# Optimization experiments

Measured on AMD Instinct MI355X. Metric: run time of the kernel, lower is better.

## Reference

```python
import jax, jax.numpy as jnp
import numpy as np

D = 1024
H = 16
S = 2048
B = 4
DF = 4 * D
EPS = 1e-5


def setup_inputs() -> dict:
    key = jax.random.key(0)
    ks = jax.random.split(key, 12)
    sd = 0.02
    return {
        "x": jax.random.normal(ks[0], (B, S, D), dtype=jnp.float32),
        "Wq": jax.random.normal(ks[1], (D, D), dtype=jnp.float32) * sd,
        "Wk": jax.random.normal(ks[2], (D, D), dtype=jnp.float32) * sd,
        "Wv": jax.random.normal(ks[3], (D, D), dtype=jnp.float32) * sd,
        "Wo": jax.random.normal(ks[4], (D, D), dtype=jnp.float32) * sd,
        "bo": jnp.zeros((D,), dtype=jnp.float32),
        "W1": jax.random.normal(ks[5], (D, DF), dtype=jnp.float32) * sd,
        "b1": jnp.zeros((DF,), dtype=jnp.float32),
        "W2": jax.random.normal(ks[6], (DF, D), dtype=jnp.float32) * sd,
        "b2": jnp.zeros((D,), dtype=jnp.float32),
        "g1": jnp.ones((D,), dtype=jnp.float32),
        "s1": jnp.zeros((D,), dtype=jnp.float32),
        "g2": jnp.ones((D,), dtype=jnp.float32),
        "s2": jnp.zeros((D,), dtype=jnp.float32),
    }


def _gelu(x):
    # tanh approximation exactly as in the torch GELU module
    c = jnp.sqrt(jnp.asarray(2.0 / jnp.pi, dtype=x.dtype))
    return 0.5 * x * (1.0 + jnp.tanh(c * (x + 0.044715 * x ** 3)))


def _layernorm(x, scale, shift):
    mean = jnp.mean(x, axis=-1, keepdims=True)
    var = jnp.var(x, axis=-1, keepdims=True)  # biased, as unbiased=False
    return scale * (x - mean) * jax.lax.rsqrt(var + EPS) + shift


def _attention(x, Wq, Wk, Wv, Wo, bo):
    b, s, d = x.shape
    hd = d // H
    q = (x @ Wq).reshape(b, s, H, hd).transpose(0, 2, 1, 3)  # [b,h,s,hd]
    k = (x @ Wk).reshape(b, s, H, hd).transpose(0, 2, 1, 3)
    v = (x @ Wv).reshape(b, s, H, hd).transpose(0, 2, 1, 3)
    scores = jnp.einsum("bhqd,bhkd->bhqk", q, k) / jnp.sqrt(jnp.asarray(hd, x.dtype))
    mask = jnp.triu(jnp.ones((s, s), dtype=bool), k=1)
    scores = jnp.where(mask, -jnp.inf, scores)
    w = jax.nn.softmax(scores, axis=-1)  # dropout is identity (rate=0 / eval)
    ctx = jnp.einsum("bhqk,bhkd->bhqd", w, v)
    ctx = ctx.transpose(0, 2, 1, 3).reshape(b, s, d)
    return ctx @ Wo + bo


def reference(x, Wq, Wk, Wv, Wo, bo, W1, b1, W2, b2, g1, s1, g2, s2):
    h = x + _attention(_layernorm(x, g1, s1), Wq, Wk, Wv, Wo, bo)
    y = _layernorm(h, g2, s2)
    ff = _gelu(y @ W1 + b1) @ W2 + b2
    return h + ff
```

## Files before the change

### kernel.cpp

```cpp
#include <hip/hip_runtime.h>
#include <hip/hip_bf16.h>

#define DEV __device__ __forceinline__

typedef __bf16 bf16x8 __attribute__((ext_vector_type(8)));
typedef __bf16 bf16x2v __attribute__((ext_vector_type(2)));
typedef float f32x4 __attribute__((ext_vector_type(4)));
typedef float f32x16 __attribute__((ext_vector_type(16)));
typedef unsigned int u32;
typedef unsigned int u32x4 __attribute__((ext_vector_type(4)));
typedef __hip_bfloat16 hbf;

constexpr int Dm = 1024;
constexpr int Hh = 16;
constexpr int Ss = 2048;
constexpr int Bb = 4;
constexpr int DFm = 4096;
constexpr int LDQ = 3072;

DEV unsigned short f2bfu(float f) {
  hbf h = __float2bfloat16(f);
  return __builtin_bit_cast(unsigned short, h);
}

DEV float bfu2f(unsigned short u) { return __builtin_bit_cast(float, (u32)u << 16); }

DEV u32 pkbf(float x, float y) {
  bf16x2v v = {(__bf16)x, (__bf16)y};
  return __builtin_bit_cast(u32, v);
}

DEV float gelu_f(float x) {
  float e = __expf(-1.5957691216057308f * (x + 0.044715f * x * x * x));
  return x * __builtin_amdgcn_rcpf(1.f + e);
}

template <int N>
DEV void s_vmcnt() {
  if constexpr (N == 0) asm volatile("s_waitcnt vmcnt(0)" ::: "memory");
  else if constexpr (N == 5) asm volatile("s_waitcnt vmcnt(5)" ::: "memory");
  else if constexpr (N == 6) asm volatile("s_waitcnt vmcnt(6)" ::: "memory");
  else if constexpr (N == 8) asm volatile("s_waitcnt vmcnt(8)" ::: "memory");
  else static_assert(N == 0, "unsupported vmcnt");
}

#define GLDS(src, dst)                                                                     \
  __builtin_amdgcn_global_load_lds((const __attribute__((address_space(1))) void*)(src),   \
                                   (__attribute__((address_space(3))) void*)(dst), 16, 0, 0)

__global__ __launch_bounds__(256) void wtransall_kernel(
    const float* __restrict__ Wq, const float* __restrict__ Wk,
    const float* __restrict__ Wv, const float* __restrict__ Wo,
    const float* __restrict__ W1, const float* __restrict__ W2,
    hbf* __restrict__ dqkv, hbf* __restrict__ dwo,
    hbf* __restrict__ dw1, hbf* __restrict__ dw2) {
  __shared__ float tile[32][33];
  const int i = blockIdx.x;
  const float* W;
  hbf* Wt;
  int K, N, k0, n0;
  if (i < 4096) {
    int z = i >> 10, j = i & 1023;
    W = z == 0 ? Wq : z == 1 ? Wk : z == 2 ? Wv : Wo;
    Wt = z == 3 ? dwo : dqkv + (size_t)z * 1024 * 1024;
    K = 1024; N = 1024; k0 = (j & 31) * 32; n0 = (j >> 5) * 32;
  } else if (i < 8192) {
    int j = i - 4096;
    W = W1; Wt = dw1; K = 1024; N = 4096;
    k0 = (j & 31) * 32; n0 = (j >> 5) * 32;
  } else {
    int j = i - 8192;
    W = W2; Wt = dw2; K = 4096; N = 1024;
    k0 = (j & 127) * 32; n0 = (j >> 7) * 32;
  }
  int tx = threadIdx.x & 31, ty = threadIdx.x >> 5;
  for (int r = ty; r < 32; r += 8) tile[r][tx] = W[(size_t)(k0 + r) * N + n0 + tx];
  __syncthreads();
  for (int r = ty; r < 32; r += 8)
    Wt[(size_t)(n0 + r) * K + k0 + tx] = __float2bfloat16(tile[tx][r]);
}

template <bool INBF>
__global__ __launch_bounds__(256) void ln_kernel(const void* __restrict__ xv,
                                                 const float* __restrict__ g,
                                                 const float* __restrict__ b,
                                                 hbf* __restrict__ y) {
  int row = ((blockIdx.x & 7) << 10) | (blockIdx.x >> 3);
  int t = threadIdx.x;
  float4 v;
  if constexpr (INBF) {
    ushort4 u = ((const ushort4*)((const hbf*)xv + (size_t)row * Dm))[t];
    v.x = bfu2f(u.x); v.y = bfu2f(u.y); v.z = bfu2f(u.z); v.w = bfu2f(u.w);
  } else {
    v = ((const float4*)((const float*)xv + (size_t)row * Dm))[t];
  }
  float s = v.x + v.y + v.z + v.w;
  float q = v.x * v.x + v.y * v.y + v.z * v.z + v.w * v.w;
#pragma unroll
  for (int off = 32; off > 0; off >>= 1) {
    s += __shfl_down(s, off);
    q += __shfl_down(q, off);
  }
  __shared__ float red[10];
  int wave = t >> 6, lane = t & 63;
  if (lane == 0) { red[wave] = s; red[4 + wave] = q; }
  __syncthreads();
  if (t == 0) {
    float ts = red[0] + red[1] + red[2] + red[3];
    float tq = red[4] + red[5] + red[6] + red[7];
    float mean = ts * (1.f / Dm);
    float var = tq * (1.f / Dm) - mean * mean;
    red[8] = mean;
    red[9] = rsqrtf(var + 1e-5f);
  }
  __syncthreads();
  float mean = red[8], inv = red[9];
  float4 gv = ((const float4*)g)[t];
  float4 bv = ((const float4*)b)[t];
  ushort4 o;
  o.x = f2bfu(gv.x * (v.x - mean) * inv + bv.x);
  o.y = f2bfu(gv.y * (v.y - mean) * inv + bv.y);
  o.z = f2bfu(gv.z * (v.z - mean) * inv + bv.z);
  o.w = f2bfu(gv.w * (v.w - mean) * inv + bv.w);
  ((ushort4*)(y + (size_t)row * Dm))[t] = o;
}

template <int BM, int BN, int WM, int WN, int NTHR, int NPH, int ACT, bool HAS_BIAS, int RES,
          bool OUT_BF16>
__global__ __launch_bounds__(NTHR, 2) void gemm8(const hbf* __restrict__ A,
                                                 const hbf* __restrict__ Bt,
                                                 void* __restrict__ Cv,
                                                 const float* __restrict__ bias,
                                                 const void* __restrict__ resv,
                                                 int M, int N, int K) {
  constexpr int MR = (BM / WM) / 16, NR = (BN / WN) / 16;
  constexpr int MQ = MR / 2, NQ = NR / 2;
  constexpr int RPA = (BM / WM) / 2;
  constexpr int RPB = (BN / WN) / 2;
  constexpr int ASL = (BM / 2) * 64;
  constexpr int BSL = (BN / 2) * 64;
  constexpr int PERBUF = 2 * ASL + 2 * BSL;
  constexpr int ALD = ASL / (8 * NTHR);
  constexpr int BLD = BSL / (8 * NTHR);
  constexpr int VPB = 2 * ALD + BLD;
  constexpr int VP4 = 2 * ALD + 2 * BLD;

  __shared__ __align__(16) hbf lds[2 * PERBUF];

  const int tid = threadIdx.x;
  const int lane = tid & 63, wave = tid >> 6;
  const int wr = wave / WN, wc = wave % WN;
  const int lr = lane & 15, lg = lane >> 4;

  const int xcd = blockIdx.x & 7, oidx = blockIdx.x >> 3;
  const int gsup = oidx >> 6, r6 = oidx & 63;
  const int m0 = (xcd * 8 + (r6 >> 3)) * BM;
  const int n0 = (gsup * 8 + (r6 & 7)) * BN;

  const hbf* Ab = A + (size_t)m0 * K;
  const hbf* Bb = Bt + (size_t)n0 * K;

  f32x4 acc[MR][NR] = {};

  auto stageA = [&](int mh, int t, int p) {
#pragma unroll
    for (int l = 0; l < ALD; ++l) {
      int ci = l * NTHR + tid;
      int r = ci >> 3, c = ci & 7;
      int piece = r / RPA, rl = r % RPA;
      int grow = piece * (BM / WM) + mh * RPA + rl;
      int gk = t * 64 + ((c ^ (r & 7)) << 3);
      GLDS(Ab + (size_t)grow * K + gk, lds + p * PERBUF + mh * ASL + (size_t)ci * 8);
    }
  };
  auto stageB = [&](int nh, int t, int p) {
#pragma unroll
    for (int l = 0; l < BLD; ++l) {
      int ci = l * NTHR + tid;
      int r = ci >> 3, c = ci & 7;
      int piece = r / RPB, rl = r % RPB;
      int grow = piece * (BN / WN) + nh * RPB + rl;
      int gk = t * 64 + ((c ^ (r & 7)) << 3);
      GLDS(Bb + (size_t)grow * K + gk, lds + p * PERBUF + 2 * ASL + nh * BSL + (size_t)ci * 8);
    }
  };
  auto ldA = [&](bf16x8 (&af)[MQ][2], int mh, int p) {
    const hbf* base = lds + p * PERBUF + mh * ASL;
#pragma unroll
    for (int i = 0; i < MQ; ++i)
#pragma unroll
      for (int ks = 0; ks < 2; ++ks) {
        int row = wr * RPA + i * 16 + lr;
        int slot = (ks * 4 + lg) ^ (lr & 7);
        af[i][ks] = *(const bf16x8*)(base + (size_t)row * 64 + slot * 8);
      }
  };
  auto ldAfull = [&](bf16x8 (&af)[MR][2], int p) {
#pragma unroll
    for (int f = 0; f < MR; ++f)
#pragma unroll
      for (int ks = 0; ks < 2; ++ks) {
        int mh = f >> 1, i = f & 1;
        const hbf* base = lds + p * PERBUF + mh * ASL;
        int row = wr * RPA + i * 16 + lr;
        int slot = (ks * 4 + lg) ^ (lr & 7);
        af[f][ks] = *(const bf16x8*)(base + (size_t)row * 64 + slot * 8);
      }
  };
  auto ldB = [&](bf16x8 (&bf)[NQ][2], int nh, int p) {
    const hbf* base = lds + p * PERBUF + 2 * ASL + nh * BSL;
#pragma unroll
    for (int j = 0; j < NQ; ++j)
#pragma unroll
      for (int ks = 0; ks < 2; ++ks) {
        int row = wc * RPB + j * 16 + lr;
        int slot = (ks * 4 + lg) ^ (lr & 7);
        bf[j][ks] = *(const bf16x8*)(base + (size_t)row * 64 + slot * 8);
      }
  };

#define SYNC_LGKM()                                        \
  do {                                                     \
    __builtin_amdgcn_s_barrier();                          \
    asm volatile("s_waitcnt lgkmcnt(0)" ::: "memory");     \
    __builtin_amdgcn_sched_barrier(0);                     \
  } while (0)

#define MFMA_Q(av, bv, mh, nh)                                                        \
  do {                                                                                \
    __builtin_amdgcn_s_setprio(1);                                                    \
    _Pragma("unroll") for (int i_ = 0; i_ < MQ; ++i_)                                 \
    _Pragma("unroll") for (int j_ = 0; j_ < NQ; ++j_)                                 \
    _Pragma("unroll") for (int k_ = 0; k_ < 2; ++k_)                                  \
      acc[(mh) * MQ + i_][(nh) * NQ + j_] = __builtin_amdgcn_mfma_f32_16x16x32_bf16(  \
          (av)[i_][k_], (bv)[j_][k_], acc[(mh) * MQ + i_][(nh) * NQ + j_], 0, 0, 0);  \
    __builtin_amdgcn_s_setprio(0);                                                    \
  } while (0)

#define MFMA_H(av, bv, nh)                                                            \
  do {                                                                                \
    __builtin_amdgcn_s_setprio(1);                                                    \
    _Pragma("unroll") for (int f_ = 0; f_ < MR; ++f_)                                 \
    _Pragma("unroll") for (int j_ = 0; j_ < NQ; ++j_)                                 \
    _Pragma("unroll") for (int k_ = 0; k_ < 2; ++k_)                                  \
      acc[f_][(nh) * NQ + j_] = __builtin_amdgcn_mfma_f32_16x16x32_bf16(              \
          (av)[f_][k_], (bv)[j_][k_], acc[f_][(nh) * NQ + j_], 0, 0, 0);              \
    __builtin_amdgcn_s_setprio(0);                                                    \
  } while (0)

  const int T = K >> 6;

  if constexpr (NPH == 4) {
    stageA(0, 0, 0); stageB(0, 0, 0); stageA(1, 0, 0); stageB(1, 0, 0);
    stageA(0, 1, 1); stageB(0, 1, 1); stageA(1, 1, 1); stageB(1, 1, 1);
    s_vmcnt<VP4>();
    __builtin_amdgcn_s_barrier();

    for (int t = 0; t < T; ++t) {
      const int p = t & 1;
      bf16x8 a0[MQ][2], a1[MQ][2], b0[NQ][2], b1[NQ][2];
      ldA(a0, 0, p);
      ldB(b0, 0, p);
      asm volatile("s_waitcnt lgkmcnt(8)" ::: "memory");
      SYNC_LGKM();
      MFMA_Q(a0, b0, 0, 0);
      __builtin_amdgcn_s_barrier();
      ldA(a1, 1, p);
      if (t + 2 < T) { stageA(0, t + 2, p); stageB(0, t + 2, p); }
      SYNC_LGKM();
      MFMA_Q(a1, b0, 1, 0);
      __builtin_amdgcn_s_barrier();
      ldB(b1, 1, p);
      if (t + 2 < T) stageA(1, t + 2, p);
      SYNC_LGKM();
      MFMA_Q(a1, b1, 1, 1);
      __builtin_amdgcn_s_barrier();
      if (t + 2 < T) stageB(1, t + 2, p);
      MFMA_Q(a0, b1, 0, 1);
      if (t + 1 < T) {
        if (t + 2 < T) s_vmcnt<VP4>();
        else s_vmcnt<0>();
      }
      __builtin_amdgcn_s_barrier();
    }
  } else {
    stageA(0, 0, 0); stageA(1, 0, 0); stageB(0, 0, 0); stageB(1, 0, 0);
    stageA(0, 1, 1); stageA(1, 1, 1); stageB(0, 1, 1);
    s_vmcnt<VPB>();
    __builtin_amdgcn_s_barrier();

    for (int t = 0; t < T; ++t) {
      const int p = t & 1;
      bf16x8 af[MR][2], b0[NQ][2], b1[NQ][2];
      ldAfull(af, p);
      ldB(b0, 0, p);
      if (t + 1 < T) stageB(1, t + 1, p ^ 1);
      asm volatile("s_waitcnt lgkmcnt(8)" ::: "memory");
      SYNC_LGKM();
      MFMA_H(af, b0, 0);
      __builtin_amdgcn_s_barrier();
      ldB(b1, 1, p);
      if (t + 2 < T) { stageA(0, t + 2, p); stageA(1, t + 2, p); stageB(0, t + 2, p); }
      SYNC_LGKM();
      MFMA_H(af, b1, 1);
      if (t + 1 < T) {
        if (t + 2 < T) s_vmcnt<VPB>();
        else s_vmcnt<0>();
      }
      __builtin_amdgcn_s_barrier();
    }
  }
#undef SYNC_LGKM
#undef MFMA_Q
#undef MFMA_H

#pragma unroll
  for (int mf = 0; mf < MR; ++mf) {
    int row = m0 + wr * (BM / WM) + mf * 16 + lg * 4;
#pragma unroll
    for (int n = 0; n < NR; ++n) {
      int col = n0 + wc * (BN / WN) + n * 16 + lr;
      float bvl = HAS_BIAS ? bias[col] : 0.f;
#pragma unroll
      for (int j = 0; j < 4; ++j) {
        float v = acc[mf][n][j] + bvl;
        if (ACT == 1) v = gelu_f(v);
        if constexpr (RES == 1) v += ((const float*)resv)[(size_t)(row + j) * N + col];
        else if constexpr (RES == 2)
          v += bfu2f(__builtin_bit_cast(unsigned short,
                                        ((const hbf*)resv)[(size_t)(row + j) * N + col]));
        if (OUT_BF16) ((hbf*)Cv)[(size_t)(row + j) * N + col] = __float2bfloat16(v);
        else ((float*)Cv)[(size_t)(row + j) * N + col] = v;
      }
    }
  }
}

__global__ __launch_bounds__(256) void vtrans_kernel(const hbf* __restrict__ qkv,
                                                     hbf* __restrict__ vt) {
  __shared__ unsigned short tile[64][65];
  int bh = blockIdx.y, b = bh >> 4, hh = bh & 15;
  int s0 = blockIdx.x * 64;
  int d = threadIdx.x & 63, r0 = threadIdx.x >> 6;
#pragma unroll
  for (int i = 0; i < 16; ++i) {
    int r = r0 * 16 + i;
    tile[d][r] = __builtin_bit_cast(unsigned short,
                                    qkv[(size_t)(b * Ss + s0 + r) * LDQ + 2048 + hh * 64 + d]);
  }
  __syncthreads();
#pragma unroll
  for (int i = 0; i < 16; ++i) {
    int r = r0 * 16 + i;
    vt[(size_t)(bh * 64 + r) * Ss + s0 + d] = __builtin_bit_cast(hbf, tile[r][d]);
  }
}

__global__ __launch_bounds__(256, 3) void attn_kernel(const hbf* __restrict__ qkv,
                                                      const hbf* __restrict__ vt,
                                                      hbf* __restrict__ ctx) {
  __shared__ __align__(16) hbf Ks[2][64 * 64];
  __shared__ __align__(16) hbf Vs[2][64 * 64];

  const int tid = threadIdx.x;
  const int wave = tid >> 6, lane = tid & 63;
  const int l31 = lane & 31, hi = lane >> 5;

  const int gi = blockIdx.x;
  const int xslot = gi & 7, kk = gi >> 3;
  const int rank = kk >> 3, hg = kk & 7;
  const int bh = hg * 8 + xslot;
  const int bx = 15 - rank;
  const int b = bh >> 4, hh = bh & 15;
  const int q0b = bx * 128;
  const int q0w = q0b + wave * 32;
  const int nsteps = (q0b + 128) >> 6;
  const int my_steps = (q0w + 95) >> 6;

  constexpr float QSCALE = 0.18033688011112042f;
  bf16x8 qf[4];
  {
    const hbf* qrow = qkv + (size_t)(b * Ss + q0w + l31) * LDQ + hh * 64 + hi * 8;
#pragma unroll
    for (int ds = 0; ds < 4; ++ds) {
      bf16x8 t = *(const bf16x8*)(qrow + ds * 16);
#pragma unroll
      for (int e = 0; e < 8; ++e) qf[ds][e] = (__bf16)((float)t[e] * QSCALE);
    }
  }

  const hbf* kbase = qkv + 1024 + (size_t)(b * Ss) * LDQ + hh * 64;
  const hbf* vbase = vt + (size_t)(bh * 64) * Ss;
  const int i0 = tid, i1 = tid + 256;
  const int r0 = i0 >> 3, s0c = (i0 & 7), r1 = i1 >> 3, s1c = (i1 & 7);
  const int c0 = 8 * (s0c ^ (r0 & 7)), c1 = 8 * (s1c ^ (r1 & 7));

  f32x16 ot[2] = {};
  float m_run = -1e30f, l_run = 0.f;

  {
    hbf* kd = &Ks[0][0];
    hbf* vd = &Vs[0][0];
    GLDS(kbase + (size_t)r0 * LDQ + c0, kd + i0 * 8);
    GLDS(kbase + (size_t)r1 * LDQ + c1, kd + i1 * 8);
    GLDS(vbase + (size_t)r0 * Ss + c0, vd + i0 * 8);
    GLDS(vbase + (size_t)r1 * Ss + c1, vd + i1 * 8);
  }
  __syncthreads();

  int buf = 0;
  for (int it = 0; it < nsteps; ++it) {
    const int k0 = it << 6;
    if (it + 1 < nsteps) {
      hbf* kd = &Ks[buf ^ 1][0];
      hbf* vd = &Vs[buf ^ 1][0];
      GLDS(kbase + (size_t)(k0 + 64 + r0) * LDQ + c0, kd + i0 * 8);
      GLDS(kbase + (size_t)(k0 + 64 + r1) * LDQ + c1, kd + i1 * 8);
      GLDS(vbase + (size_t)r0 * Ss + k0 + 64 + c0, vd + i0 * 8);
      GLDS(vbase + (size_t)r1 * Ss + k0 + 64 + c1, vd + i1 * 8);
    }

    if (it < my_steps) {
      const hbf* kt = &Ks[buf][0];
      f32x16 st[2] = {};
      __builtin_amdgcn_s_setprio(1);
#pragma unroll
      for (int c = 0; c < 2; ++c) {
        const int krow = l31 + 32 * c;
        const int kr7 = krow & 7;
#pragma unroll
        for (int ds = 0; ds < 4; ++ds) {
          bf16x8 kf = *(const bf16x8*)(kt + krow * 64 + 8 * ((ds * 2 + hi) ^ kr7));
          st[c] = __builtin_amdgcn_mfma_f32_32x32x16_bf16(kf, qf[ds], st[c], 0, 0, 0);
        }
      }
      __builtin_amdgcn_s_setprio(0);

      if (it == my_steps - 1) {
        const int qg = q0w + l31;
#pragma unroll
        for (int c = 0; c < 2; ++c)
#pragma unroll
          for (int rg = 0; rg < 16; ++rg) {
            int kg = k0 + c * 32 + (rg & 3) + 8 * (rg >> 2) + 4 * hi;
            if (kg > qg) st[c][rg] = -3e38f;
          }
      }

      float mx = -3e38f;
#pragma unroll
      for (int c = 0; c < 2; ++c)
#pragma unroll
        for (int rg = 0; rg < 16; ++rg) mx = fmaxf(mx, st[c][rg]);
      mx = fmaxf(mx, __shfl_xor(mx, 32));
      if (!__all(mx - m_run <= 11.541560327111707f)) {
        float mn = fmaxf(m_run, mx);
        float sc = exp2f(m_run - mn);
        m_run = mn;
        l_run *= sc;
#pragma unroll
        for (int dc = 0; dc < 2; ++dc)
#pragma unroll
          for (int rg = 0; rg < 16; ++rg) ot[dc][rg] *= sc;
      }
      float rs = 0.f;
#pragma unroll
      for (int c = 0; c < 2; ++c)
#pragma unroll
        for (int rg = 0; rg < 16; ++rg) {
          float p = exp2f(st[c][rg] - m_run);
          st[c][rg] = p;
          rs += p;
        }
      rs += __shfl_xor(rs, 32);
      l_run += rs;

      bf16x8 pf[2][2];
#pragma unroll
      for (int c = 0; c < 2; ++c)
#pragma unroll
        for (int ks = 0; ks < 2; ++ks) {
          const int rb = ks * 8;
          u32 a0 = pkbf(st[c][rb + 0], st[c][rb + 1]);
          u32 a1 = pkbf(st[c][rb + 2], st[c][rb + 3]);
          u32 b0 = pkbf(st[c][rb + 4], st[c][rb + 5]);
          u32 b1 = pkbf(st[c][rb + 6], st[c][rb + 7]);
          u32 pa0 = __shfl_xor(a0, 32), pa1 = __shfl_xor(a1, 32);
          u32 pb0 = __shfl_xor(b0, 32), pb1 = __shfl_xor(b1, 32);
          u32x4 f;
          f.x = hi ? pb0 : a0;
          f.y = hi ? pb1 : a1;
          f.z = hi ? b0 : pa0;
          f.w = hi ? b1 : pa1;
          pf[c][ks] = __builtin_bit_cast(bf16x8, f);
        }

      const hbf* vtl = &Vs[buf][0];
      __builtin_amdgcn_s_setprio(1);
#pragma unroll
      for (int dc = 0; dc < 2; ++dc) {
        const int vrow = l31 + 32 * dc;
        const int vr7 = vrow & 7;
#pragma unroll
        for (int c = 0; c < 2; ++c)
#pragma unroll
          for (int ks = 0; ks < 2; ++ks) {
            bf16x8 vf = *(const bf16x8*)(vtl + vrow * 64 + 8 * ((c * 4 + ks * 2 + hi) ^ vr7));
            ot[dc] = __builtin_amdgcn_mfma_f32_32x32x16_bf16(vf, pf[c][ks], ot[dc], 0, 0, 0);
          }
      }
      __builtin_amdgcn_s_setprio(0);
    }

    __syncthreads();
    buf ^= 1;
  }

  const float inv = __builtin_amdgcn_rcpf(l_run);
  hbf* crow = ctx + (size_t)(b * Ss + q0w + l31) * Dm + hh * 64;
#pragma unroll
  for (int dc = 0; dc < 2; ++dc)
#pragma unroll
    for (int rg = 0; rg < 4; ++rg) {
      ushort4 w;
      w.x = f2bfu(ot[dc][rg * 4 + 0] * inv);
      w.y = f2bfu(ot[dc][rg * 4 + 1] * inv);
      w.z = f2bfu(ot[dc][rg * 4 + 2] * inv);
      w.w = f2bfu(ot[dc][rg * 4 + 3] * inv);
      *(ushort4*)(crow + dc * 32 + rg * 8 + hi * 4) = w;
    }
}

extern "C" void kernel_launch(void* const* d_in, const int* in_sizes, int n_in,
                              void* d_out, int out_size, void* d_ws, size_t ws_size,
                              hipStream_t stream) {
  const float* x  = (const float*)d_in[0];
  const float* Wq = (const float*)d_in[1];
  const float* Wk = (const float*)d_in[2];
  const float* Wv = (const float*)d_in[3];
  const float* Wo = (const float*)d_in[4];
  const float* bo = (const float*)d_in[5];
  const float* W1 = (const float*)d_in[6];
  const float* b1 = (const float*)d_in[7];
  const float* W2 = (const float*)d_in[8];
  const float* b2 = (const float*)d_in[9];
  const float* g1 = (const float*)d_in[10];
  const float* s1 = (const float*)d_in[11];
  const float* g2 = (const float*)d_in[12];
  const float* s2 = (const float*)d_in[13];
  float* out = (float*)d_out;

  char* ws = (char*)d_ws;
  constexpr size_t MB = 1024ull * 1024ull;
  hbf* wqkvT = (hbf*)(ws + 0 * MB);
  hbf* woT   = (hbf*)(ws + 6 * MB);
  hbf* w1T   = (hbf*)(ws + 8 * MB);
  hbf* w2T   = (hbf*)(ws + 16 * MB);
  hbf* xln   = (hbf*)(ws + 24 * MB);
  hbf* ctx   = (hbf*)(ws + 24 * MB);
  hbf* y2    = (hbf*)(ws + 24 * MB);
  hbf* qkvb  = (hbf*)(ws + 40 * MB);
  hbf* vtb   = (hbf*)(ws + 88 * MB);
  hbf* ff1   = (hbf*)(ws + 40 * MB);
  hbf* hbb   = (hbf*)(ws + 104 * MB);
  (void)ws_size; (void)in_sizes; (void)n_in; (void)out_size;

  const int BS = Bb * Ss;

  wtransall_kernel<<<12288, 256, 0, stream>>>(Wq, Wk, Wv, Wo, W1, W2,
                                              wqkvT, woT, w1T, w2T);

  ln_kernel<false><<<BS, 256, 0, stream>>>(x, g1, s1, xln);

  gemm8<128, 128, 2, 2, 256, 2, 0, false, 0, true><<<1536, 256, 0, stream>>>(
      xln, wqkvT, qkvb, nullptr, nullptr, BS, LDQ, Dm);

  vtrans_kernel<<<dim3(Ss / 64, Bb * Hh), 256, 0, stream>>>(qkvb, vtb);

  attn_kernel<<<dim3(1024), 256, 0, stream>>>(qkvb, vtb, ctx);

  gemm8<128, 128, 2, 2, 256, 2, 0, true, 1, true><<<512, 256, 0, stream>>>(
      ctx, woT, hbb, bo, x, BS, Dm, Dm);

  ln_kernel<true><<<BS, 256, 0, stream>>>(hbb, g2, s2, y2);

  gemm8<128, 128, 2, 2, 256, 2, 1, true, 0, true><<<2048, 256, 0, stream>>>(
      y2, w1T, ff1, b1, nullptr, BS, DFm, Dm);

  gemm8<128, 128, 2, 2, 256, 2, 0, true, 2, false><<<512, 256, 0, stream>>>(
      ff1, w2T, out, b2, hbb, BS, Dm, DFm);
}
```

Before: 343.9 us.

## Fuse LN1 into weight prep and V transpose into QKV GEMM epilogue

Merges the first LayerNorm into the weight-transpose prep kernel as extra blocks, so one launch does both. The QKV GEMM epilogue now writes the V columns directly in transposed layout, which removes the separate vtrans kernel and its extra read and write of V. It also raises the attention kernel's launch-bounds occupancy hint from 3 to 4 blocks per CU. The costs are fewer registers available to attention and scattered 8-byte stores in the GEMM epilogue for the V part.

```diff
diff --git a/kernel.cpp b/kernel.cpp
--- a/kernel.cpp
+++ b/kernel.cpp
@@ -48,52 +48,85 @@
   __builtin_amdgcn_global_load_lds((const __attribute__((address_space(1))) void*)(src),   \
                                    (__attribute__((address_space(3))) void*)(dst), 16, 0, 0)
 
-__global__ __launch_bounds__(256) void wtransall_kernel(
+__global__ __launch_bounds__(256) void prep_kernel(
     const float* __restrict__ Wq, const float* __restrict__ Wk,
     const float* __restrict__ Wv, const float* __restrict__ Wo,
     const float* __restrict__ W1, const float* __restrict__ W2,
     hbf* __restrict__ dqkv, hbf* __restrict__ dwo,
-    hbf* __restrict__ dw1, hbf* __restrict__ dw2) {
-  __shared__ float tile[32][33];
+    hbf* __restrict__ dw1, hbf* __restrict__ dw2,
+    const float* __restrict__ x, const float* __restrict__ g1,
+    const float* __restrict__ s1, hbf* __restrict__ xln) {
   const int i = blockIdx.x;
-  const float* W;
-  hbf* Wt;
-  int K, N, k0, n0;
-  if (i < 4096) {
-    int z = i >> 10, j = i & 1023;
-    W = z == 0 ? Wq : z == 1 ? Wk : z == 2 ? Wv : Wo;
-    Wt = z == 3 ? dwo : dqkv + (size_t)z * 1024 * 1024;
-    K = 1024; N = 1024; k0 = (j & 31) * 32; n0 = (j >> 5) * 32;
-  } else if (i < 8192) {
-    int j = i - 4096;
-    W = W1; Wt = dw1; K = 1024; N = 4096;
-    k0 = (j & 31) * 32; n0 = (j >> 5) * 32;
+  if (i < 12288) {
+    __shared__ float tile[32][33];
+    const float* W;
+    hbf* Wt;
+    int K, N, k0, n0;
+    if (i < 4096) {
+      int z = i >> 10, j = i & 1023;
+      W = z == 0 ? Wq : z == 1 ? Wk : z == 2 ? Wv : Wo;
+      Wt = z == 3 ? dwo : dqkv + (size_t)z * 1024 * 1024;
+      K = 1024; N = 1024; k0 = (j & 31) * 32; n0 = (j >> 5) * 32;
+    } else if (i < 8192) {
+      int j = i - 4096;
+      W = W1; Wt = dw1; K = 1024; N = 4096;
+      k0 = (j & 31) * 32; n0 = (j >> 5) * 32;
+    } else {
+      int j = i - 8192;
+      W = W2; Wt = dw2; K = 4096; N = 1024;
+      k0 = (j & 127) * 32; n0 = (j >> 7) * 32;
+    }
+    int tx = threadIdx.x & 31, ty = threadIdx.x >> 5;
+    for (int r = ty; r < 32; r += 8) tile[r][tx] = W[(size_t)(k0 + r) * N + n0 + tx];
+    __syncthreads();
+    for (int r = ty; r < 32; r += 8)
+      Wt[(size_t)(n0 + r) * K + k0 + tx] = __float2bfloat16(tile[tx][r]);
   } else {
-    int j = i - 8192;
-    W = W2; Wt = dw2; K = 4096; N = 1024;
-    k0 = (j & 127) * 32; n0 = (j >> 7) * 32;
-  }
-  int tx = threadIdx.x & 31, ty = threadIdx.x >> 5;
-  for (int r = ty; r < 32; r += 8) tile[r][tx] = W[(size_t)(k0 + r) * N + n0 + tx];
-  __syncthreads();
-  for (int r = ty; r < 32; r += 8)
-    Wt[(size_t)(n0 + r) * K + k0 + tx] = __float2bfloat16(tile[tx][r]);
-}
-
-template <bool INBF>
-__global__ __launch_bounds__(256) void ln_kernel(const void* __restrict__ xv,
+    const int bid = i - 12288;
+    int row = ((bid & 7) << 10) | (bid >> 3);
+    int t = threadIdx.x;
+    float4 v = ((const float4*)(x + (size_t)row * Dm))[t];
+    float s = v.x + v.y + v.z + v.w;
+    float q = v.x * v.x + v.y * v.y + v.z * v.z + v.w * v.w;
+#pragma unroll
+    for (int off = 32; off > 0; off >>= 1) {
+      s += __shfl_down(s, off);
+      q += __shfl_down(q, off);
+    }
+    __shared__ float red[10];
+    int wave = t >> 6, lane = t & 63;
+    if (lane == 0) { red[wave] = s; red[4 + wave] = q; }
+    __syncthreads();
+    if (t == 0) {
+      float ts = red[0] + red[1] + red[2] + red[3];
+      float tq = red[4] + red[5] + red[6] + red[7];
+      float mean = ts * (1.f / Dm);
+      float var = tq * (1.f / Dm) - mean * mean;
+      red[8] = mean;
+      red[9] = rsqrtf(var + 1e-5f);
+    }
+    __syncthreads();
+    float mean = red[8], inv = red[9];
+    float4 gv = ((const float4*)g1)[t];
+    float4 bv = ((const float4*)s1)[t];
+    ushort4 o;
+    o.x = f2bfu(gv.x * (v.x - mean) * inv + bv.x);
+    o.y = f2bfu(gv.y * (v.y - mean) * inv + bv.y);
+    o.z = f2bfu(gv.z * (v.z - mean) * inv + bv.z);
+    o.w = f2bfu(gv.w * (v.w - mean) * inv + bv.w);
+    ((ushort4*)(xln + (size_t)row * Dm))[t] = o;
+  }
+}
+
+__global__ __launch_bounds__(256) void ln_kernel(const hbf* __restrict__ xv,
                                                  const float* __restrict__ g,
                                                  const float* __restrict__ b,
                                                  hbf* __restrict__ y) {
   int row = ((blockIdx.x & 7) << 10) | (blockIdx.x >> 3);
   int t = threadIdx.x;
   float4 v;
-  if constexpr (INBF) {
-    ushort4 u = ((const ushort4*)((const hbf*)xv + (size_t)row * Dm))[t];
-    v.x = bfu2f(u.x); v.y = bfu2f(u.y); v.z = bfu2f(u.z); v.w = bfu2f(u.w);
-  } else {
-    v = ((const float4*)((const float*)xv + (size_t)row * Dm))[t];
-  }
+  ushort4 u = ((const ushort4*)(xv + (size_t)row * Dm))[t];
+  v.x = bfu2f(u.x); v.y = bfu2f(u.y); v.z = bfu2f(u.z); v.w = bfu2f(u.w);
   float s = v.x + v.y + v.z + v.w;
   float q = v.x * v.x + v.y * v.y + v.z * v.z + v.w * v.w;
 #pragma unroll
@@ -126,12 +159,13 @@
 }
 
 template <int BM, int BN, int WM, int WN, int NTHR, int NPH, int ACT, bool HAS_BIAS, int RES,
-          bool OUT_BF16>
+          bool OUT_BF16, int VTR>
 __global__ __launch_bounds__(NTHR, 2) void gemm8(const hbf* __restrict__ A,
                                                  const hbf* __restrict__ Bt,
                                                  void* __restrict__ Cv,
                                                  const float* __restrict__ bias,
                                                  const void* __restrict__ resv,
+                                                 hbf* __restrict__ vtrout,
                                                  int M, int N, int K) {
   constexpr int MR = (BM / WM) / 16, NR = (BN / WN) / 16;
   constexpr int MQ = MR / 2, NQ = NR / 2;
@@ -184,17 +218,6 @@
       GLDS(Bb + (size_t)grow * K + gk, lds + p * PERBUF + 2 * ASL + nh * BSL + (size_t)ci * 8);
     }
   };
-  auto ldA = [&](bf16x8 (&af)[MQ][2], int mh, int p) {
-    const hbf* base = lds + p * PERBUF + mh * ASL;
-#pragma unroll
-    for (int i = 0; i < MQ; ++i)
-#pragma unroll
-      for (int ks = 0; ks < 2; ++ks) {
-        int row = wr * RPA + i * 16 + lr;
-        int slot = (ks * 4 + lg) ^ (lr & 7);
-        af[i][ks] = *(const bf16x8*)(base + (size_t)row * 64 + slot * 8);
-      }
-  };
   auto ldAfull = [&](bf16x8 (&af)[MR][2], int p) {
 #pragma unroll
     for (int f = 0; f < MR; ++f)
@@ -205,6 +228,17 @@
         int row = wr * RPA + i * 16 + lr;
         int slot = (ks * 4 + lg) ^ (lr & 7);
         af[f][ks] = *(const bf16x8*)(base + (size_t)row * 64 + slot * 8);
+      }
+  };
+  auto ldA = [&](bf16x8 (&af)[MQ][2], int mh, int p) {
+    const hbf* base = lds + p * PERBUF + mh * ASL;
+#pragma unroll
+    for (int i = 0; i < MQ; ++i)
+#pragma unroll
+      for (int ks = 0; ks < 2; ++ks) {
+        int row = wr * RPA + i * 16 + lr;
+        int slot = (ks * 4 + lg) ^ (lr & 7);
+        af[i][ks] = *(const bf16x8*)(base + (size_t)row * 64 + slot * 8);
       }
   };
   auto ldB = [&](bf16x8 (&bf)[NQ][2], int nh, int p) {
@@ -321,6 +355,7 @@
     for (int n = 0; n < NR; ++n) {
       int col = n0 + wc * (BN / WN) + n * 16 + lr;
       float bvl = HAS_BIAS ? bias[col] : 0.f;
+      float tv[4];
 #pragma unroll
       for (int j = 0; j < 4; ++j) {
         float v = acc[mf][n][j] + bvl;
@@ -329,34 +364,28 @@
         else if constexpr (RES == 2)
           v += bfu2f(__builtin_bit_cast(unsigned short,
                                         ((const hbf*)resv)[(size_t)(row + j) * N + col]));
-        if (OUT_BF16) ((hbf*)Cv)[(size_t)(row + j) * N + col] = __float2bfloat16(v);
-        else ((float*)Cv)[(size_t)(row + j) * N + col] = v;
-      }
-    }
-  }
-}
-
-__global__ __launch_bounds__(256) void vtrans_kernel(const hbf* __restrict__ qkv,
-                                                     hbf* __restrict__ vt) {
-  __shared__ unsigned short tile[64][65];
-  int bh = blockIdx.y, b = bh >> 4, hh = bh & 15;
-  int s0 = blockIdx.x * 64;
-  int d = threadIdx.x & 63, r0 = threadIdx.x >> 6;
-#pragma unroll
-  for (int i = 0; i < 16; ++i) {
-    int r = r0 * 16 + i;
-    tile[d][r] = __builtin_bit_cast(unsigned short,
-                                    qkv[(size_t)(b * Ss + s0 + r) * LDQ + 2048 + hh * 64 + d]);
-  }
-  __syncthreads();
-#pragma unroll
-  for (int i = 0; i < 16; ++i) {
-    int r = r0 * 16 + i;
-    vt[(size_t)(bh * 64 + r) * Ss + s0 + d] = __builtin_bit_cast(hbf, tile[r][d]);
-  }
-}
-
-__global__ __launch_bounds__(256, 3) void attn_kernel(const hbf* __restrict__ qkv,
+        tv[j] = v;
+      }
+      if constexpr (VTR != 0) {
+        if (col >= 2048) {
+          ushort4 w;
+          w.x = f2bfu(tv[0]); w.y = f2bfu(tv[1]); w.z = f2bfu(tv[2]); w.w = f2bfu(tv[3]);
+          int bb = row >> 11;
+          size_t vrow = (size_t)(bb * 1024 + col - 2048);
+          *(ushort4*)((unsigned short*)vtrout + vrow * Ss + (row & 2047)) = w;
+          continue;
+        }
+      }
+#pragma unroll
+      for (int j = 0; j < 4; ++j) {
+        if (OUT_BF16) ((hbf*)Cv)[(size_t)(row + j) * N + col] = __float2bfloat16(tv[j]);
+        else ((float*)Cv)[(size_t)(row + j) * N + col] = tv[j];
+      }
+    }
+  }
+}
+
+__global__ __launch_bounds__(256, 4) void attn_kernel(const hbf* __restrict__ qkv,
                                                       const hbf* __restrict__ vt,
                                                       hbf* __restrict__ ctx) {
   __shared__ __align__(16) hbf Ks[2][64 * 64];
@@ -567,26 +596,22 @@
 
   const int BS = Bb * Ss;
 
-  wtransall_kernel<<<12288, 256, 0, stream>>>(Wq, Wk, Wv, Wo, W1, W2,
-                                              wqkvT, woT, w1T, w2T);
-
-  ln_kernel<false><<<BS, 256, 0, stream>>>(x, g1, s1, xln);
-
-  gemm8<128, 128, 2, 2, 256, 2, 0, false, 0, true><<<1536, 256, 0, stream>>>(
-      xln, wqkvT, qkvb, nullptr, nullptr, BS, LDQ, Dm);
-
-  vtrans_kernel<<<dim3(Ss / 64, Bb * Hh), 256, 0, stream>>>(qkvb, vtb);
+  prep_kernel<<<20480, 256, 0, stream>>>(Wq, Wk, Wv, Wo, W1, W2,
+                                         wqkvT, woT, w1T, w2T, x, g1, s1, xln);
+
+  gemm8<128, 128, 2, 2, 256, 2, 0, false, 0, true, 1><<<1536, 256, 0, stream>>>(
+      xln, wqkvT, qkvb, nullptr, nullptr, vtb, BS, LDQ, Dm);
 
   attn_kernel<<<dim3(1024), 256, 0, stream>>>(qkvb, vtb, ctx);
 
-  gemm8<128, 128, 2, 2, 256, 2, 0, true, 1, true><<<512, 256, 0, stream>>>(
-      ctx, woT, hbb, bo, x, BS, Dm, Dm);
-
-  ln_kernel<true><<<BS, 256, 0, stream>>>(hbb, g2, s2, y2);
-
-  gemm8<128, 128, 2, 2, 256, 2, 1, true, 0, true><<<2048, 256, 0, stream>>>(
-      y2, w1T, ff1, b1, nullptr, BS, DFm, Dm);
-
-  gemm8<128, 128, 2, 2, 256, 2, 0, true, 2, false><<<512, 256, 0, stream>>>(
-      ff1, w2T, out, b2, hbb, BS, Dm, DFm);
-}
+  gemm8<128, 128, 2, 2, 256, 2, 0, true, 1, true, 0><<<512, 256, 0, stream>>>(
+      ctx, woT, hbb, bo, x, nullptr, BS, Dm, Dm);
+
+  ln_kernel<<<BS, 256, 0, stream>>>(hbb, g2, s2, y2);
+
+  gemm8<128, 128, 2, 2, 256, 2, 1, true, 0, true, 0><<<2048, 256, 0, stream>>>(
+      y2, w1T, ff1, b1, nullptr, nullptr, BS, DFm, Dm);
+
+  gemm8<128, 128, 2, 2, 256, 2, 0, true, 2, false, 0><<<512, 256, 0, stream>>>(
+      ff1, w2T, out, b2, hbb, nullptr, BS, Dm, DFm);
+}
```

New measurement: 335.1 us. 1.03x faster.
